# Kernel optimization log

Measured on AMD Instinct MI355X. Metric: run time of the kernel, lower is better.

Reference implementation:

```python
import jax, jax.numpy as jnp
import numpy as np

HIDDEN_DIM = 2048
NUM_HEADS = 16
HEAD_DIM = HIDDEN_DIM // NUM_HEADS
BATCH = 2
SEQ = 2048


def setup_inputs() -> dict:
    key = jax.random.key(0)
    ks = jax.random.split(key, 5)
    scale = 1.0 / np.sqrt(HIDDEN_DIM)
    x = jax.random.normal(ks[0], (BATCH, SEQ, HIDDEN_DIM), dtype=jnp.float32)
    w_q = jax.random.normal(ks[1], (HIDDEN_DIM, HIDDEN_DIM), dtype=jnp.float32) * scale
    w_k = jax.random.normal(ks[2], (HIDDEN_DIM, HIDDEN_DIM), dtype=jnp.float32) * scale
    w_v = jax.random.normal(ks[3], (HIDDEN_DIM, HIDDEN_DIM), dtype=jnp.float32) * scale
    w_o = jax.random.normal(ks[4], (HIDDEN_DIM, HIDDEN_DIM), dtype=jnp.float32) * scale
    return {"x": x, "w_q": w_q, "w_k": w_k, "w_v": w_v, "w_o": w_o}


def reference(x, w_q, w_k, w_v, w_o):
    # Projections: x @ W.T  (weights stored as (out, in) like torch)
    q = jnp.einsum('bsd,ed->bse', x, w_q)
    k = jnp.einsum('bsd,ed->bse', x, w_k)
    v = jnp.einsum('bsd,ed->bse', x, w_v)
    b, s, _ = q.shape
    # split heads: (b, h, s, hd)
    q = q.reshape(b, s, NUM_HEADS, HEAD_DIM).transpose(0, 2, 1, 3)
    k = k.reshape(b, s, NUM_HEADS, HEAD_DIM).transpose(0, 2, 1, 3)
    v = v.reshape(b, s, NUM_HEADS, HEAD_DIM).transpose(0, 2, 1, 3)
    scale = 1.0 / np.sqrt(HEAD_DIM)
    # Online-softmax tiling in the source (causal=False default) is
    # mathematically identical to standard softmax attention.
    scores = jnp.einsum('bhqd,bhkd->bhqk', q, k) * scale
    p = jax.nn.softmax(scores, axis=-1)
    o = jnp.einsum('bhqk,bhkd->bhqd', p, v)
    o = o.transpose(0, 2, 1, 3).reshape(b, s, HIDDEN_DIM)
    return jnp.einsum('bsd,ed->bse', o, w_o)
```

## Files before the change

kernel.cpp:

```cpp
#include <hip/hip_runtime.h>


typedef _Float16 half8 __attribute__((ext_vector_type(8)));
typedef _Float16 half4 __attribute__((ext_vector_type(4)));
typedef float floatx4 __attribute__((ext_vector_type(4)));

__device__ __forceinline__ void async16(const void* g, void* l) {
  __builtin_amdgcn_global_load_lds((__attribute__((address_space(1))) void*)(g),
                                   (__attribute__((address_space(3))) void*)(l),
                                   16, 0, 0);
}

__global__ void cvt_all(const float* __restrict__ x, const float* __restrict__ w0,
                        const float* __restrict__ w1, const float* __restrict__ w2,
                        const float* __restrict__ w3, _Float16* __restrict__ xh,
                        _Float16* __restrict__ wh, float scale0) {
  int i = blockIdx.x * blockDim.x + threadIdx.x;
  const int XQ = 1 << 21;
  float sc = 1.0f;
  const float* src;
  _Float16* dst;
  int j;
  if (i < XQ) { src = x; dst = xh; j = i; }
  else {
    int t = i - XQ;
    int m = t >> 20;
    src = (m == 0) ? w0 : (m == 1) ? w1 : (m == 2) ? w2 : w3;
    if (m == 0) sc = scale0;
    dst = wh; j = t;
  }
  int js = (i < XQ) ? j : (j & ((1 << 20) - 1));
  float4 v = reinterpret_cast<const float4*>(src)[js];
  union { _Float16 h[4]; short4 s; } u;
  u.h[0] = (_Float16)(v.x * sc); u.h[1] = (_Float16)(v.y * sc);
  u.h[2] = (_Float16)(v.z * sc); u.h[3] = (_Float16)(v.w * sc);
  reinterpret_cast<short4*>(dst)[j] = u.s;
}

__device__ __forceinline__ void rdA4(half8 (&f)[4][2], const _Float16* base,
                                     int ch0, int ch1) {
#pragma unroll
  for (int mt = 0; mt < 4; ++mt) {
    f[mt][0] = *reinterpret_cast<const half8*>(base + mt * 2048 + ch0);
    f[mt][1] = *reinterpret_cast<const half8*>(base + mt * 2048 + ch1);
  }
}
__device__ __forceinline__ void rdB2(half8 (&f)[2][2], const _Float16* base,
                                     int ch0, int ch1) {
#pragma unroll
  for (int nt = 0; nt < 2; ++nt) {
    f[nt][0] = *reinterpret_cast<const half8*>(base + nt * 4096 + ch0);
    f[nt][1] = *reinterpret_cast<const half8*>(base + nt * 4096 + ch1);
  }
}
template <int MO, int NO>
__device__ __forceinline__ void mmg16(floatx4 (&acc)[8][4], const half8 (&af)[4][2],
                                      const half8 (&bf)[2][2]) {
#pragma unroll
  for (int kk = 0; kk < 2; ++kk)
#pragma unroll
    for (int mt = 0; mt < 4; ++mt)
#pragma unroll
      for (int nt = 0; nt < 2; ++nt)
        acc[MO + mt][NO + nt] = __builtin_amdgcn_mfma_f32_16x16x32_f16(
            af[mt][kk], bf[nt][kk], acc[MO + mt][NO + nt], 0, 0, 0);
}

template <int OUT_MODE, int NBN>
__global__ __launch_bounds__(512, 2)
void gemm_nt(const _Float16* __restrict__ A, const _Float16* __restrict__ Bw,
             void* __restrict__ Cv, void* __restrict__ Cv2) {
  __shared__ _Float16 As[2][256 * 64];
  __shared__ _Float16 Bs[2][256 * 64];
  const int tid = threadIdx.x;
  const int wave = tid >> 6, lane = tid & 63;
  const int wm = wave >> 2, wn = wave & 3;
  const int l15 = lane & 15, l4 = lane >> 4;

  const int nwg = NBN * 16;
  const int orig = blockIdx.x;
  const int swz = (orig & 7) * (nwg >> 3) + (orig >> 3);
  const int bn = swz % NBN, bm = swz / NBN;

  const int srow = tid >> 3;
  const int g = (tid & 7) ^ (srow & 7);
  const _Float16* ags = A + (size_t)(bm * 256 + srow) * 2048 + g * 8;
  const _Float16* bgs = Bw + (size_t)(bn * 256 + srow) * 2048 + g * 8;
  const int ldst = tid * 8;

  const int arow = wm * 16 + l15;
  const int brow = wn * 16 + l15;
  const int ch0 = (l4 ^ (l15 & 7)) * 8;
  const int ch1 = ((l4 + 4) ^ (l15 & 7)) * 8;

#pragma unroll
  for (int j = 0; j < 4; ++j) {
    async16(ags + (size_t)j * 131072, &As[0][j * 4096 + ldst]);
    async16(bgs + (size_t)j * 131072, &Bs[0][j * 4096 + ldst]);
  }
  asm volatile("s_waitcnt vmcnt(0)" ::: "memory");
  __builtin_amdgcn_s_barrier();

  floatx4 acc[8][4] = {};
  half8 afA[4][2], afB[4][2], bfA[2][2], bfB[2][2];

  for (int t = 0; t < 31; ++t) {
    const int cur = t & 1, nxt = cur ^ 1;
    const int kn = t * 64 + 64;
    const _Float16* Ab = &As[cur][arow * 64];
    const _Float16* Bb = &Bs[cur][brow * 64];
    _Float16* Asn = &As[nxt][ldst];
    _Float16* Bsn = &Bs[nxt][ldst];

    rdA4(afA, Ab, ch0, ch1);
    async16(ags + kn, Asn);
    async16(ags + 131072 + kn, Asn + 4096);
    __builtin_amdgcn_s_barrier();
    __builtin_amdgcn_s_waitcnt(0xC07F);
    __builtin_amdgcn_s_setprio(1);
    if (t) mmg16<4, 2>(acc, afB, bfB);
    __builtin_amdgcn_s_setprio(0);
    asm volatile("s_waitcnt vmcnt(6)" ::: "memory");
    __builtin_amdgcn_s_barrier();

    rdB2(bfA, Bb, ch0, ch1);
    async16(bgs + kn, Bsn);
    async16(bgs + 131072 + kn, Bsn + 4096);
    __builtin_amdgcn_s_barrier();
    __builtin_amdgcn_s_waitcnt(0xC07F);
    __builtin_amdgcn_s_setprio(1);
    mmg16<0, 0>(acc, afA, bfA);
    __builtin_amdgcn_s_setprio(0);
    asm volatile("s_waitcnt vmcnt(6)" ::: "memory");
    __builtin_amdgcn_s_barrier();

    rdB2(bfB, Bb + 8192, ch0, ch1);
    async16(bgs + 262144 + kn, Bsn + 8192);
    async16(bgs + 393216 + kn, Bsn + 12288);
    __builtin_amdgcn_s_barrier();
    __builtin_amdgcn_s_waitcnt(0xC07F);
    __builtin_amdgcn_s_setprio(1);
    mmg16<0, 2>(acc, afA, bfB);
    __builtin_amdgcn_s_setprio(0);
    asm volatile("s_waitcnt vmcnt(6)" ::: "memory");
    __builtin_amdgcn_s_barrier();

    rdA4(afB, Ab + 8192, ch0, ch1);
    async16(ags + 262144 + kn, Asn + 8192);
    async16(ags + 393216 + kn, Asn + 12288);
    __builtin_amdgcn_s_barrier();
    __builtin_amdgcn_s_waitcnt(0xC07F);
    __builtin_amdgcn_s_setprio(1);
    mmg16<4, 0>(acc, afB, bfA);
    __builtin_amdgcn_s_setprio(0);
    asm volatile("s_waitcnt vmcnt(6)" ::: "memory");
    __builtin_amdgcn_s_barrier();
  }

  {
    const _Float16* Ab = &As[1][arow * 64];
    const _Float16* Bb = &Bs[1][brow * 64];
    rdA4(afA, Ab, ch0, ch1);
    mmg16<4, 2>(acc, afB, bfB);
    asm volatile("s_waitcnt vmcnt(4)" ::: "memory");
    __builtin_amdgcn_s_barrier();
    rdB2(bfA, Bb, ch0, ch1);
    mmg16<0, 0>(acc, afA, bfA);
    asm volatile("s_waitcnt vmcnt(2)" ::: "memory");
    __builtin_amdgcn_s_barrier();
    rdB2(bfB, Bb + 8192, ch0, ch1);
    mmg16<0, 2>(acc, afA, bfB);
    asm volatile("s_waitcnt vmcnt(0)" ::: "memory");
    __builtin_amdgcn_s_barrier();
    rdA4(afB, Ab + 8192, ch0, ch1);
    mmg16<4, 0>(acc, afB, bfA);
    mmg16<4, 2>(acc, afB, bfB);
  }

  const int cb0 = bn * 256;
  if constexpr (OUT_MODE == 0) {
    if (cb0 < 4096) {
      _Float16* C = (_Float16*)Cv + (size_t)(cb0 >> 11) * (4096ull * 2048);
#pragma unroll
      for (int mt = 0; mt < 8; ++mt)
#pragma unroll
        for (int nt = 0; nt < 4; ++nt) {
          int r0 = bm * 256 + mt * 32 + wm * 16 + l4 * 4;
          int cg = (cb0 + nt * 64 + wn * 16 + l15) & 2047;
#pragma unroll
          for (int r = 0; r < 4; ++r)
            C[(size_t)(r0 + r) * 2048 + cg] = (_Float16)acc[mt][nt][r];
        }
    } else {
      _Float16* C = (_Float16*)Cv2;
#pragma unroll
      for (int mt = 0; mt < 8; ++mt)
#pragma unroll
        for (int nt = 0; nt < 4; ++nt) {
          int m0 = bm * 256 + mt * 32 + wm * 16 + l4 * 4;
          int d = cb0 + nt * 64 + wn * 16 + l15 - 4096;
          size_t base = (size_t)(m0 >> 11) * (2048ull * 2048) + (size_t)d * 2048 + (m0 & 2047);
          union { _Float16 h[4]; short4 s; } u;
#pragma unroll
          for (int r = 0; r < 4; ++r) u.h[r] = (_Float16)acc[mt][nt][r];
          *reinterpret_cast<short4*>(C + base) = u.s;
        }
    }
  } else {
    float* C = (float*)Cv;
#pragma unroll
    for (int mt = 0; mt < 8; ++mt)
#pragma unroll
      for (int nt = 0; nt < 4; ++nt) {
        int r0 = bm * 256 + mt * 32 + wm * 16 + l4 * 4;
        int cg = cb0 + nt * 64 + wn * 16 + l15;
#pragma unroll
        for (int r = 0; r < 4; ++r)
          C[(size_t)(r0 + r) * 2048 + cg] = acc[mt][nt][r];
      }
  }
}

__global__ __launch_bounds__(256, 2)
void flash_attn(const _Float16* __restrict__ Q, const _Float16* __restrict__ Kg,
                const _Float16* __restrict__ Vt, _Float16* __restrict__ O) {
  __shared__ _Float16 Ks[64 * 128];
  __shared__ _Float16 Vs[128 * 64];
  __shared__ _Float16 Ps[128 * 64];
  const int tid = threadIdx.x, wave = tid >> 6, lane = tid & 63;
  const int l15 = lane & 15, l4 = lane >> 4;
  const int bh = blockIdx.y, b = bh >> 4, h = bh & 15;
  const int q0 = blockIdx.x * 128;

  const _Float16* Qp = Q + ((size_t)(b * 2048 + q0 + wave * 32)) * 2048 + h * 128;
  const _Float16* Kp = Kg + (size_t)b * 2048 * 2048 + h * 128;
  const _Float16* Vp = Vt + (size_t)b * 2048 * 2048 + (size_t)(h * 128) * 2048;

  half8 qf[2][4];
#pragma unroll
  for (int qt = 0; qt < 2; ++qt)
#pragma unroll
    for (int ks = 0; ks < 4; ++ks)
      qf[qt][ks] = *reinterpret_cast<const half8*>(
          Qp + (size_t)(qt * 16 + l15) * 2048 + ks * 32 + l4 * 8);

  floatx4 oacc[2][8] = {};
  float lsumq[2] = {0.f, 0.f};

  for (int k0 = 0; k0 < 2048; k0 += 64) {
    __syncthreads();
#pragma unroll
    for (int i = 0; i < 4; ++i) {
      int c = i * 256 + tid;
      int row = c >> 4, cc = c & 15;
      int g = cc ^ (row & 15);
      async16(Kp + (size_t)(k0 + row) * 2048 + g * 8, &Ks[c * 8]);
    }
#pragma unroll
    for (int i = 0; i < 4; ++i) {
      int c = i * 256 + tid;
      int row = c >> 3, cc = c & 7;
      int g = cc ^ (row & 7);
      async16(Vp + (size_t)row * 2048 + k0 + g * 8, &Vs[c * 8]);
    }
    __syncthreads();

    floatx4 sacc[4][2] = {};
#pragma unroll
    for (int ks = 0; ks < 4; ++ks) {
      half8 kf[4];
#pragma unroll
      for (int st = 0; st < 4; ++st) {
        int row = st * 16 + l15;
        int ch = (ks * 4 + l4) ^ l15;
        kf[st] = *reinterpret_cast<const half8*>(&Ks[row * 128 + ch * 8]);
      }
#pragma unroll
      for (int st = 0; st < 4; ++st)
#pragma unroll
        for (int qt = 0; qt < 2; ++qt)
          sacc[st][qt] = __builtin_amdgcn_mfma_f32_16x16x32_f16(kf[st], qf[qt][ks], sacc[st][qt], 0, 0, 0);
    }

#pragma unroll
    for (int qt = 0; qt < 2; ++qt)
#pragma unroll
      for (int st = 0; st < 4; ++st) {
        float p0 = exp2f(sacc[st][qt][0]);
        float p1 = exp2f(sacc[st][qt][1]);
        float p2 = exp2f(sacc[st][qt][2]);
        float p3 = exp2f(sacc[st][qt][3]);
        lsumq[qt] += (p0 + p1) + (p2 + p3);
        half4 pv;
        pv[0] = (_Float16)p0; pv[1] = (_Float16)p1;
        pv[2] = (_Float16)p2; pv[3] = (_Float16)p3;
        int ch = (st * 2 + (l4 >> 1)) ^ (l15 & 7);
        *reinterpret_cast<half4*>(
            &Ps[(wave * 32 + qt * 16 + l15) * 64 + ch * 8 + (l4 & 1) * 4]) = pv;
      }

    __builtin_amdgcn_s_waitcnt(0xC07F);

#pragma unroll
    for (int ks2 = 0; ks2 < 2; ++ks2) {
      half8 pf[2];
#pragma unroll
      for (int mt = 0; mt < 2; ++mt)
        pf[mt] = *reinterpret_cast<const half8*>(
            &Ps[(wave * 32 + mt * 16 + l15) * 64 + (((ks2 * 4 + l4) ^ (l15 & 7)) * 8)]);
#pragma unroll
      for (int nt2 = 0; nt2 < 8; ++nt2) {
        int row = nt2 * 16 + l15;
        int ch = (ks2 * 4 + l4) ^ (row & 7);
        half8 vf = *reinterpret_cast<const half8*>(&Vs[row * 64 + ch * 8]);
#pragma unroll
        for (int mt = 0; mt < 2; ++mt)
          oacc[mt][nt2] = __builtin_amdgcn_mfma_f32_16x16x32_f16(pf[mt], vf, oacc[mt][nt2], 0, 0, 0);
      }
    }
  }

#pragma unroll
  for (int qt = 0; qt < 2; ++qt) {
    lsumq[qt] += __shfl_xor(lsumq[qt], 16);
    lsumq[qt] += __shfl_xor(lsumq[qt], 32);
  }

  _Float16* Op = O + ((size_t)(b * 2048 + q0 + wave * 32)) * 2048 + h * 128;
#pragma unroll
  for (int mt = 0; mt < 2; ++mt)
#pragma unroll
    for (int r = 0; r < 4; ++r) {
      float inv = 1.0f / __shfl(lsumq[mt], l4 * 4 + r);
#pragma unroll
      for (int nt2 = 0; nt2 < 8; ++nt2) {
        int row = mt * 16 + l4 * 4 + r;
        int col = nt2 * 16 + l15;
        Op[(size_t)row * 2048 + col] = (_Float16)(oacc[mt][nt2][r] * inv);
      }
    }
}

extern "C" void kernel_launch(void* const* d_in, const int* in_sizes, int n_in,
                              void* d_out, int out_size, void* d_ws, size_t ws_size,
                              hipStream_t stream) {
  const float* x = (const float*)d_in[0];
  const float* wq = (const float*)d_in[1];
  const float* wk = (const float*)d_in[2];
  const float* wv = (const float*)d_in[3];
  const float* wo = (const float*)d_in[4];
  float* out = (float*)d_out;

  const size_t XN = (size_t)4096 * 2048;
  const size_t WN = (size_t)2048 * 2048;
  _Float16* xh = (_Float16*)d_ws;
  _Float16* qh = xh + XN;
  _Float16* vth = xh + 3 * XN;
  _Float16* oh = xh + 4 * XN;
  _Float16* wqh = xh + 5 * XN;

  const float SM_SCALE = 0.08838834764831845f * 1.4426950408889634f;

  cvt_all<<<dim3(24576), 256, 0, stream>>>(x, wq, wk, wv, wo, xh, wqh, SM_SCALE);
  gemm_nt<0, 24><<<dim3(384), 512, 0, stream>>>(xh, wqh, qh, vth);
  flash_attn<<<dim3(16, 32), 256, 0, stream>>>(qh, qh + XN, vth, oh);
  gemm_nt<2, 8><<<dim3(128), 512, 0, stream>>>(oh, wqh + 3 * WN, out, nullptr);
}
```

Baseline: 403.2 us.

## Split-K output projection with atomics and reorder GEMM LDS reads in pipeline

The output projection GEMM now splits K in two across 256 workgroups instead of 128, accumulating into a zeroed output with float atomic adds, so more of the chip's compute units are busy. The main GEMM loop is also reorganised: both A and B fragments are read earlier, and the LDS waitcnts are replaced by sched_barriers with different vmcnt thresholds, to overlap LDS reads with MFMA work. The split-K path adds a memset and atomic traffic and makes the summation order nondeterministic. The loosened waits could also race on LDS reads.

```diff
diff --git a/kernel.cpp b/kernel.cpp
--- a/kernel.cpp
+++ b/kernel.cpp
@@ -66,7 +66,7 @@
             af[mt][kk], bf[nt][kk], acc[MO + mt][NO + nt], 0, 0, 0);
 }
 
-template <int OUT_MODE, int NBN>
+template <int OUT_MODE, int NBN, int KT>
 __global__ __launch_bounds__(512, 2)
 void gemm_nt(const _Float16* __restrict__ A, const _Float16* __restrict__ Bw,
              void* __restrict__ Cv, void* __restrict__ Cv2) {
@@ -77,15 +77,22 @@
   const int wm = wave >> 2, wn = wave & 3;
   const int l15 = lane & 15, l4 = lane >> 4;
 
-  const int nwg = NBN * 16;
-  const int orig = blockIdx.x;
-  const int swz = (orig & 7) * (nwg >> 3) + (orig >> 3);
-  const int bn = swz % NBN, bm = swz / NBN;
+  int bm, bn, koff;
+  if constexpr (OUT_MODE == 3) {
+    const int bid = blockIdx.x;
+    const int kh = bid & 1, t2 = bid >> 1;
+    const int swz = (t2 & 7) * 16 + (t2 >> 3);
+    bn = swz & 7; bm = swz >> 3; koff = kh * 1024;
+  } else {
+    const int nwg = NBN * 16;
+    const int swz = (blockIdx.x & 7) * (nwg >> 3) + (blockIdx.x >> 3);
+    bn = swz % NBN; bm = swz / NBN; koff = 0;
+  }
 
   const int srow = tid >> 3;
   const int g = (tid & 7) ^ (srow & 7);
-  const _Float16* ags = A + (size_t)(bm * 256 + srow) * 2048 + g * 8;
-  const _Float16* bgs = Bw + (size_t)(bn * 256 + srow) * 2048 + g * 8;
+  const _Float16* ags = A + (size_t)(bm * 256 + srow) * 2048 + koff + g * 8;
+  const _Float16* bgs = Bw + (size_t)(bn * 256 + srow) * 2048 + koff + g * 8;
   const int ldst = tid * 8;
 
   const int arow = wm * 16 + l15;
@@ -104,7 +111,8 @@
   floatx4 acc[8][4] = {};
   half8 afA[4][2], afB[4][2], bfA[2][2], bfB[2][2];
 
-  for (int t = 0; t < 31; ++t) {
+#pragma unroll 2
+  for (int t = 0; t < KT - 1; ++t) {
     const int cur = t & 1, nxt = cur ^ 1;
     const int kn = t * 64 + 64;
     const _Float16* Ab = &As[cur][arow * 64];
@@ -113,47 +121,46 @@
     _Float16* Bsn = &Bs[nxt][ldst];
 
     rdA4(afA, Ab, ch0, ch1);
+    rdB2(bfA, Bb, ch0, ch1);
     async16(ags + kn, Asn);
     async16(ags + 131072 + kn, Asn + 4096);
-    __builtin_amdgcn_s_barrier();
-    __builtin_amdgcn_s_waitcnt(0xC07F);
+    __builtin_amdgcn_sched_barrier(0);
+    __builtin_amdgcn_s_barrier();
     __builtin_amdgcn_s_setprio(1);
     if (t) mmg16<4, 2>(acc, afB, bfB);
     __builtin_amdgcn_s_setprio(0);
-    asm volatile("s_waitcnt vmcnt(6)" ::: "memory");
-    __builtin_amdgcn_s_barrier();
-
-    rdB2(bfA, Bb, ch0, ch1);
+    asm volatile("s_waitcnt vmcnt(4)" ::: "memory");
+    __builtin_amdgcn_s_barrier();
+
+    rdB2(bfB, Bb + 8192, ch0, ch1);
     async16(bgs + kn, Bsn);
     async16(bgs + 131072 + kn, Bsn + 4096);
-    __builtin_amdgcn_s_barrier();
-    __builtin_amdgcn_s_waitcnt(0xC07F);
+    __builtin_amdgcn_sched_barrier(0);
+    __builtin_amdgcn_s_barrier();
     __builtin_amdgcn_s_setprio(1);
     mmg16<0, 0>(acc, afA, bfA);
     __builtin_amdgcn_s_setprio(0);
-    asm volatile("s_waitcnt vmcnt(6)" ::: "memory");
-    __builtin_amdgcn_s_barrier();
-
-    rdB2(bfB, Bb + 8192, ch0, ch1);
+    asm volatile("s_waitcnt vmcnt(4)" ::: "memory");
+    __builtin_amdgcn_s_barrier();
+
+    rdA4(afB, Ab + 8192, ch0, ch1);
     async16(bgs + 262144 + kn, Bsn + 8192);
     async16(bgs + 393216 + kn, Bsn + 12288);
-    __builtin_amdgcn_s_barrier();
-    __builtin_amdgcn_s_waitcnt(0xC07F);
+    __builtin_amdgcn_sched_barrier(0);
+    __builtin_amdgcn_s_barrier();
     __builtin_amdgcn_s_setprio(1);
     mmg16<0, 2>(acc, afA, bfB);
     __builtin_amdgcn_s_setprio(0);
-    asm volatile("s_waitcnt vmcnt(6)" ::: "memory");
-    __builtin_amdgcn_s_barrier();
-
-    rdA4(afB, Ab + 8192, ch0, ch1);
+    __builtin_amdgcn_s_barrier();
+
     async16(ags + 262144 + kn, Asn + 8192);
     async16(ags + 393216 + kn, Asn + 12288);
-    __builtin_amdgcn_s_barrier();
-    __builtin_amdgcn_s_waitcnt(0xC07F);
+    __builtin_amdgcn_sched_barrier(0);
+    __builtin_amdgcn_s_barrier();
     __builtin_amdgcn_s_setprio(1);
     mmg16<4, 0>(acc, afB, bfA);
     __builtin_amdgcn_s_setprio(0);
-    asm volatile("s_waitcnt vmcnt(6)" ::: "memory");
+    asm volatile("s_waitcnt vmcnt(4)" ::: "memory");
     __builtin_amdgcn_s_barrier();
   }
 
@@ -161,18 +168,17 @@
     const _Float16* Ab = &As[1][arow * 64];
     const _Float16* Bb = &Bs[1][brow * 64];
     rdA4(afA, Ab, ch0, ch1);
+    rdB2(bfA, Bb, ch0, ch1);
+    __builtin_amdgcn_s_barrier();
     mmg16<4, 2>(acc, afB, bfB);
-    asm volatile("s_waitcnt vmcnt(4)" ::: "memory");
-    __builtin_amdgcn_s_barrier();
-    rdB2(bfA, Bb, ch0, ch1);
+    asm volatile("s_waitcnt vmcnt(2)" ::: "memory");
+    __builtin_amdgcn_s_barrier();
+    rdB2(bfB, Bb + 8192, ch0, ch1);
     mmg16<0, 0>(acc, afA, bfA);
-    asm volatile("s_waitcnt vmcnt(2)" ::: "memory");
-    __builtin_amdgcn_s_barrier();
-    rdB2(bfB, Bb + 8192, ch0, ch1);
+    asm volatile("s_waitcnt vmcnt(0)" ::: "memory");
+    __builtin_amdgcn_s_barrier();
+    rdA4(afB, Ab + 8192, ch0, ch1);
     mmg16<0, 2>(acc, afA, bfB);
-    asm volatile("s_waitcnt vmcnt(0)" ::: "memory");
-    __builtin_amdgcn_s_barrier();
-    rdA4(afB, Ab + 8192, ch0, ch1);
     mmg16<4, 0>(acc, afB, bfA);
     mmg16<4, 2>(acc, afB, bfB);
   }
@@ -206,7 +212,7 @@
           *reinterpret_cast<short4*>(C + base) = u.s;
         }
     }
-  } else {
+  } else if constexpr (OUT_MODE == 2) {
     float* C = (float*)Cv;
 #pragma unroll
     for (int mt = 0; mt < 8; ++mt)
@@ -217,6 +223,18 @@
 #pragma unroll
         for (int r = 0; r < 4; ++r)
           C[(size_t)(r0 + r) * 2048 + cg] = acc[mt][nt][r];
+      }
+  } else {
+    float* C = (float*)Cv;
+#pragma unroll
+    for (int mt = 0; mt < 8; ++mt)
+#pragma unroll
+      for (int nt = 0; nt < 4; ++nt) {
+        int r0 = bm * 256 + mt * 32 + wm * 16 + l4 * 4;
+        int cg = cb0 + nt * 64 + wn * 16 + l15;
+#pragma unroll
+        for (int r = 0; r < 4; ++r)
+          unsafeAtomicAdd(&C[(size_t)(r0 + r) * 2048 + cg], acc[mt][nt][r]);
       }
   }
 }
@@ -362,7 +380,8 @@
   const float SM_SCALE = 0.08838834764831845f * 1.4426950408889634f;
 
   cvt_all<<<dim3(24576), 256, 0, stream>>>(x, wq, wk, wv, wo, xh, wqh, SM_SCALE);
-  gemm_nt<0, 24><<<dim3(384), 512, 0, stream>>>(xh, wqh, qh, vth);
+  hipMemsetAsync(out, 0, (size_t)4096 * 2048 * 4, stream);
+  gemm_nt<0, 24, 32><<<dim3(384), 512, 0, stream>>>(xh, wqh, qh, vth);
   flash_attn<<<dim3(16, 32), 256, 0, stream>>>(qh, qh + XN, vth, oh);
-  gemm_nt<2, 8><<<dim3(128), 512, 0, stream>>>(oh, wqh + 3 * WN, out, nullptr);
-}
+  gemm_nt<3, 8, 16><<<dim3(256), 512, 0, stream>>>(oh, wqh + 3 * WN, out, nullptr);
+}
```

Result: slower. 430.1 us (+6.7%).
